# Kernel tuning notes

Measured on AMD Instinct MI355X. Metric: run time of the kernel, lower is better.

## Reference

```python
import jax, jax.numpy as jnp
import numpy as np

BLOCK_SIZE = 1024
OUTLIER_SIGMA = 3.0
OUT_FEATURES = 11008
IN_FEATURES = 4096
TOKENS = 64


def _quantize_mixed_np(W):
    """Faithful numpy port of quantize_mixed (BLOCK_SIZE divides numel exactly here)."""
    flat = W.astype(np.float32).reshape(-1)
    nb = flat.size // BLOCK_SIZE
    blocks = flat.reshape(nb, BLOCK_SIZE)
    mu = blocks.mean(axis=1, keepdims=True)
    sig = np.maximum(blocks.std(axis=1, ddof=1, keepdims=True), 1e-8)  # torch.std is unbiased
    outlier = np.abs(blocks - mu) > OUTLIER_SIGMA * sig
    abs_max = np.maximum(np.abs(np.where(outlier, 0.0, blocks)).max(axis=1), 1e-8)
    scales = (abs_max / 127.0).astype(np.float16)
    q = np.clip(np.round(blocks / abs_max[:, None] * 127.0), -127, 127).astype(np.int8)
    all_pos = np.arange(nb, dtype=np.int64)[:, None] * BLOCK_SIZE + np.arange(BLOCK_SIZE, dtype=np.int64)[None, :]
    int8_data = q[~outlier]                      # row-major == torch order
    fp16_data = blocks[outlier].astype(np.float16)
    int8_pos = all_pos[~outlier].astype(np.int32)
    fp16_pos = all_pos[outlier].astype(np.int32)
    block_idx = np.nonzero(~outlier)[0].astype(np.int32)  # block index per int8 value
    return int8_data, fp16_data, scales, int8_pos, fp16_pos, block_idx


def setup_inputs() -> dict:
    key = jax.random.key(0)
    k_x, k_b = jax.random.split(key)
    rng = np.random.default_rng(0)
    W = (rng.standard_normal((OUT_FEATURES, IN_FEATURES)) * 0.02).astype(np.float32)
    int8_data, fp16_data, scales, int8_pos, fp16_pos, block_idx = _quantize_mixed_np(W)
    x = jax.random.normal(k_x, (TOKENS, IN_FEATURES), dtype=jnp.float16)
    bias = jax.random.normal(k_b, (OUT_FEATURES,), dtype=jnp.float16) * jnp.float16(0.02)
    return {
        "x": x,
        "int8_data": jnp.asarray(int8_data),
        "fp16_data": jnp.asarray(fp16_data),
        "scales": jnp.asarray(scales),
        "bias": bias,
        "int8_pos": jnp.asarray(int8_pos),
        "fp16_pos": jnp.asarray(fp16_pos),
        "block_idx": jnp.asarray(block_idx),
    }


def reference(x, int8_data, fp16_data, scales, bias, int8_pos, fp16_pos, block_idx):
    out_features = bias.shape[0]
    in_features = x.shape[1]
    numel = out_features * in_features  # divisible by BLOCK_SIZE for these dims
    # dequantize_mixed: scatter fp16 outliers and dequantized int8 values into flat fp16 buffer
    flat = jnp.zeros((numel,), dtype=jnp.float16)
    flat = flat.at[fp16_pos].set(fp16_data)
    flat = flat.at[int8_pos].set(int8_data.astype(jnp.float16) * scales[block_idx])
    W = flat.reshape(out_features, in_features)
    # F.linear(x, W, bias) in fp16
    return jnp.dot(x.astype(jnp.float16), W.T) + bias
```

## Files before the change

kernel.cpp:

```cpp
#include <hip/hip_runtime.h>
#include <hip/hip_fp16.h>

#define TOK   64
#define INF   4096
#define OUTF  11008
#define NSLC  (OUTF * INF / 64)
#define NBLK  (OUTF / 16)

typedef __attribute__((ext_vector_type(8))) _Float16 half8;
typedef __attribute__((ext_vector_type(4))) _Float16 half4;
typedef __attribute__((ext_vector_type(4))) float floatx4;

__global__ __launch_bounds__(256) void precompute_kernel(
    const float* __restrict__ x, const int* __restrict__ fppos, int nf,
    _Float16* __restrict__ x16, int* __restrict__ cum64) {
  const int t = blockIdx.x * 256 + threadIdx.x;
  if (t < (TOK * INF) / 4) {
    const floatx4 f = *(const floatx4*)&x[t * 4];
    half4 h;
    h[0] = (_Float16)f[0]; h[1] = (_Float16)f[1];
    h[2] = (_Float16)f[2]; h[3] = (_Float16)f[3];
    *(half4*)&x16[t * 4] = h;
  }
  if (t <= NSLC) {
    const int target = t << 6;
    int lo = 0, hi = nf;
    while (lo < hi) {
      const int mid = (lo + hi) >> 1;
      if (fppos[mid] < target) lo = mid + 1; else hi = mid;
    }
    cum64[t] = lo;
  }
}

__global__ __launch_bounds__(256) void fused_gemm_kernel(
    const _Float16* __restrict__ x16, const int* __restrict__ i8,
    const float* __restrict__ fpdat, const int* __restrict__ fppos,
    const float* __restrict__ scales, const float* __restrict__ bias,
    const int* __restrict__ cum64, float* __restrict__ out, int n8) {
  __shared__ float red[4 * 64 * 16];

  const int tid  = threadIdx.x;
  const int wave = tid >> 6;
  const int lane = tid & 63;
  const int quad = lane >> 4;
  const int ln   = lane & 15;
  const int n0   = blockIdx.x * 16;

  const int r = n0 + ln;
  const float s = scales[r * 4 + wave];
  const int pbase = r * INF + wave * 1024 + quad * 8;

  const _Float16* ap = &x16[ln * INF + wave * 1024 + quad * 8];

  floatx4 acc0 = {0,0,0,0}, acc1 = {0,0,0,0}, acc2 = {0,0,0,0}, acc3 = {0,0,0,0};

#pragma unroll 2
  for (int st = 0; st < 32; ++st) {
    const int p  = pbase + st * 32;
    const int sI = p >> 6;
    const int c0 = cum64[sI];
    const int c1 = cum64[sI + 1];

    int f = 0, lt = 0;
    for (int j = c0; j < c1; ++j) {
      const int d = fppos[j] - p;
      lt += (d < 0);
      f |= ((unsigned)d < 8u) ? (1 << d) : 0;
    }

    const int i0 = p - c0 - lt;
    half8 bh;
    if ((f == 0) & (i0 + 8 <= n8)) {
      int l[8];
      __builtin_memcpy(l, &i8[i0], 32);
#pragma unroll
      for (int e = 0; e < 8; ++e) bh[e] = (_Float16)((float)l[e] * s);
    } else {
      int q = i0, jo = c0 + lt;
      const int m = n8 - 1;
#pragma unroll
      for (int e = 0; e < 8; ++e) {
        const int flg = (f >> e) & 1;
        float v;
        if (flg) { v = fpdat[jo]; ++jo; }
        else     { v = (float)i8[q > m ? m : q] * s; ++q; }
        bh[e] = (_Float16)v;
      }
    }

    const int ko = st * 32;
    const half8 a0 = *(const half8*)&ap[ko];
    const half8 a1 = *(const half8*)&ap[16 * INF + ko];
    const half8 a2 = *(const half8*)&ap[32 * INF + ko];
    const half8 a3 = *(const half8*)&ap[48 * INF + ko];
    acc0 = __builtin_amdgcn_mfma_f32_16x16x32_f16(a0, bh, acc0, 0, 0, 0);
    acc1 = __builtin_amdgcn_mfma_f32_16x16x32_f16(a1, bh, acc1, 0, 0, 0);
    acc2 = __builtin_amdgcn_mfma_f32_16x16x32_f16(a2, bh, acc2, 0, 0, 0);
    acc3 = __builtin_amdgcn_mfma_f32_16x16x32_f16(a3, bh, acc3, 0, 0, 0);
  }

  const int mb = quad * 4;
#pragma unroll
  for (int i = 0; i < 4; ++i) red[wave * 1024 + (mb + i)      * 16 + ln] = acc0[i];
#pragma unroll
  for (int i = 0; i < 4; ++i) red[wave * 1024 + (16 + mb + i) * 16 + ln] = acc1[i];
#pragma unroll
  for (int i = 0; i < 4; ++i) red[wave * 1024 + (32 + mb + i) * 16 + ln] = acc2[i];
#pragma unroll
  for (int i = 0; i < 4; ++i) red[wave * 1024 + (48 + mb + i) * 16 + ln] = acc3[i];
  __syncthreads();

#pragma unroll
  for (int c2 = 0; c2 < 4; ++c2) {
    const int cell = tid + c2 * 256;
    const int mm = cell >> 4, nn = cell & 15;
    const float v = red[cell] + red[1024 + cell] + red[2048 + cell] +
                    red[3072 + cell] + bias[n0 + nn];
    out[mm * OUTF + n0 + nn] = v;
  }
}

extern "C" void kernel_launch(void* const* d_in, const int* in_sizes, int n_in,
                              void* d_out, int out_size, void* d_ws,
                              size_t ws_size, hipStream_t stream) {
  const float* x      = (const float*)d_in[0];
  const int*   i8     = (const int*)d_in[1];
  const float* fpdat  = (const float*)d_in[2];
  const float* scales = (const float*)d_in[3];
  const float* bias   = (const float*)d_in[4];
  const int*   fppos  = (const int*)d_in[6];

  char* wsp = (char*)d_ws;
  _Float16* x16   = (_Float16*)wsp;
  int*      cum64 = (int*)(wsp + (size_t)TOK * INF * sizeof(_Float16));
  float*    out   = (float*)d_out;

  const int n8 = in_sizes[1];
  const int nf = in_sizes[2];

  precompute_kernel<<<(NSLC + 256) / 256 + 1, 256, 0, stream>>>(x, fppos, nf,
                                                                x16, cum64);
  fused_gemm_kernel<<<NBLK, 256, 0, stream>>>(x16, i8, fpdat, fppos, scales,
                                              bias, cum64, out, n8);
}
```

Measured before the change: 532.7 us.

## Split K across four blocks with atomic accumulation and prefetched slice counts

Splits the K dimension of the fused dequant-GEMM across four workgroups per 16-column output tile, so the grid grows from 688 to 2752 blocks and each wave handles 8 steps instead of 32. Partial sums are combined with float atomicAdd into an output that is zeroed by a memset beforehand, and only the first K-slice adds the bias. The cum64 slice-boundary loads are also hoisted into a fully unrolled prefetch loop. The cost is the extra memset, atomic traffic and non-deterministic summation order.

After: 488.9 us. 1.09x faster.

```diff
diff --git a/kernel.cpp b/kernel.cpp
--- a/kernel.cpp
+++ b/kernel.cpp
@@ -6,6 +6,7 @@
 #define OUTF  11008
 #define NSLC  (OUTF * INF / 64)
 #define NBLK  (OUTF / 16)
+#define KSPL  4
 
 typedef __attribute__((ext_vector_type(8))) _Float16 half8;
 typedef __attribute__((ext_vector_type(4))) _Float16 half4;
@@ -45,22 +46,31 @@
   const int lane = tid & 63;
   const int quad = lane >> 4;
   const int ln   = lane & 15;
-  const int n0   = blockIdx.x * 16;
+  const int nt   = blockIdx.x >> 2;
+  const int kq   = blockIdx.x & 3;
+  const int n0   = nt * 16;
 
-  const int r = n0 + ln;
-  const float s = scales[r * 4 + wave];
-  const int pbase = r * INF + wave * 1024 + quad * 8;
+  const int r  = n0 + ln;
+  const float s = scales[r * 4 + kq];
+  const int kb = kq * 1024 + wave * 256 + quad * 8;
+  const int pbase = r * INF + kb;
 
-  const _Float16* ap = &x16[ln * INF + wave * 1024 + quad * 8];
+  const _Float16* ap = &x16[ln * INF + kb];
 
   floatx4 acc0 = {0,0,0,0}, acc1 = {0,0,0,0}, acc2 = {0,0,0,0}, acc3 = {0,0,0,0};
 
-#pragma unroll 2
-  for (int st = 0; st < 32; ++st) {
+  int c0a[8], c1a[8];
+#pragma unroll
+  for (int st = 0; st < 8; ++st) {
+    const int sI = (pbase + st * 32) >> 6;
+    c0a[st] = cum64[sI];
+    c1a[st] = cum64[sI + 1];
+  }
+
+#pragma unroll
+  for (int st = 0; st < 8; ++st) {
     const int p  = pbase + st * 32;
-    const int sI = p >> 6;
-    const int c0 = cum64[sI];
-    const int c1 = cum64[sI + 1];
+    const int c0 = c0a[st], c1 = c1a[st];
 
     int f = 0, lt = 0;
     for (int j = c0; j < c1; ++j) {
@@ -115,9 +125,9 @@
   for (int c2 = 0; c2 < 4; ++c2) {
     const int cell = tid + c2 * 256;
     const int mm = cell >> 4, nn = cell & 15;
-    const float v = red[cell] + red[1024 + cell] + red[2048 + cell] +
-                    red[3072 + cell] + bias[n0 + nn];
-    out[mm * OUTF + n0 + nn] = v;
+    float v = red[cell] + red[1024 + cell] + red[2048 + cell] + red[3072 + cell];
+    if (kq == 0) v += bias[n0 + nn];
+    atomicAdd(&out[mm * OUTF + n0 + nn], v);
   }
 }
 
@@ -139,8 +149,10 @@
   const int n8 = in_sizes[1];
   const int nf = in_sizes[2];
 
+  hipMemsetAsync(out, 0, (size_t)out_size * sizeof(float), stream);
   precompute_kernel<<<(NSLC + 256) / 256 + 1, 256, 0, stream>>>(x, fppos, nf,
                                                                 x16, cum64);
-  fused_gemm_kernel<<<NBLK, 256, 0, stream>>>(x16, i8, fpdat, fppos, scales,
-                                              bias, cum64, out, n8);
+  fused_gemm_kernel<<<NBLK * KSPL, 256, 0, stream>>>(x16, i8, fpdat, fppos,
+                                                     scales, bias, cum64, out,
+                                                     n8);
 }
```
